# Optimization experiments

Measured on AMD Instinct MI355X. Metric: run time of the kernel, lower is better.

The kernel has to match this reference:

```python
import jax, jax.numpy as jnp
import numpy as np

B, S, H, E = 4, 2048, 2048, 8

def _gelu(x):
    return jax.nn.gelu(x, approximate=False)  # torch nn.GELU default (erf)

def setup_inputs() -> dict:
    key = jax.random.key(0)
    ks = jax.random.split(key, 12)
    sc = 1.0 / np.sqrt(H)
    inp = {
        'hidden_states': jax.random.normal(ks[0], (B, S, H), jnp.float32),
        'attention_mask': jnp.ones((B, S), jnp.float32),
        # operation detector: Linear(H,H) -> GELU -> Linear(H,8)
        'Wd1': jax.random.normal(ks[1], (H, H), jnp.float32) * sc,
        'bd1': jnp.zeros((H,), jnp.float32),
        'Wd2': jax.random.normal(ks[2], (H, E), jnp.float32) * sc,
        'bd2': jnp.zeros((E,), jnp.float32),
        # 8 expert handlers, each PrecisionAdaptiveLinear(H,H) -> stacked [E,H,H]
        'We': jax.random.normal(ks[3], (E, H, H), jnp.float32) * sc,
        'be': jnp.zeros((E, H), jnp.float32),
        # precision_integration: Linear(H,H) -> GELU -> Linear(H,H)
        'Wi1': jax.random.normal(ks[4], (H, H), jnp.float32) * sc,
        'bi1': jnp.zeros((H,), jnp.float32),
        'Wi2': jax.random.normal(ks[5], (H, H), jnp.float32) * sc,
        'bi2': jnp.zeros((H,), jnp.float32),
    }
    return inp

def _kahan_sum_last(x):
    # Numerically-stable Kahan summation over the last axis (E elements).
    s = jnp.zeros_like(x[..., 0])
    c = jnp.zeros_like(s)
    for i in range(x.shape[-1]):
        y = x[..., i] - c
        t = s + y
        c = (t - s) - y
        s = t
    return s

def reference(hidden_states, attention_mask, Wd1, bd1, Wd2, bd2, We, be, Wi1, bi1, Wi2, bi2):
    h = hidden_states
    # router: softmax over 8 operation logits (safe_softmax == stable softmax)
    logits = _gelu(h @ Wd1 + bd1) @ Wd2 + bd2            # [B,S,E]
    op_w = jax.nn.softmax(logits, axis=-1)               # [B,S,E]
    # all 8 expert linears as one batched GEMM: [B,S,E,H]
    expert_out = jnp.einsum('bsh,ehk->bsek', h, We) + be
    weighted = expert_out * op_w[:, :, :, None]          # [B,S,E,H]
    # Kahan-combine over experts (move E to last axis)
    combined = _kahan_sum_last(jnp.moveaxis(weighted, 2, -1))  # [B,S,H]
    enhanced = _gelu(combined @ Wi1 + bi1) @ Wi2 + bi2   # [B,S,H]
    enhanced = enhanced * attention_mask[:, :, None]
    return enhanced
```

## Files before the change

kernel.cpp:

```cpp
#include <hip/hip_runtime.h>
#include <hip/hip_bf16.h>


#define MTOT 8192
#define HDIM 2048

typedef short bf16x8 __attribute__((ext_vector_type(8)));
typedef float f32x4  __attribute__((ext_vector_type(4)));

__device__ __forceinline__ unsigned short f2bf(float x) {
    unsigned int u = __float_as_uint(x);
    unsigned int r = (u + 0x7FFFu + ((u >> 16) & 1u)) >> 16;
    return (unsigned short)r;
}
__device__ __forceinline__ float bf2f(unsigned short u) {
    return __uint_as_float(((unsigned int)u) << 16);
}
__device__ __forceinline__ float gelu_f(float x) {
    return 0.5f * x * (1.0f + erff(x * 0.70710678118654752f));
}

__global__ void k_split_x(const float* __restrict__ x,
                          unsigned short* __restrict__ hi,
                          unsigned short* __restrict__ lo, long n) {
    long i = ((long)blockIdx.x * blockDim.x + threadIdx.x) * 4;
    long stride = (long)gridDim.x * blockDim.x * 4;
    for (; i < n; i += stride) {
        float4 v = *reinterpret_cast<const float4*>(x + i);
        ushort4 h, l;
        h.x = f2bf(v.x); l.x = f2bf(v.x - bf2f(h.x));
        h.y = f2bf(v.y); l.y = f2bf(v.y - bf2f(h.y));
        h.z = f2bf(v.z); l.z = f2bf(v.z - bf2f(h.z));
        h.w = f2bf(v.w); l.w = f2bf(v.w - bf2f(h.w));
        *reinterpret_cast<ushort4*>(hi + i) = h;
        *reinterpret_cast<ushort4*>(lo + i) = l;
    }
}

__global__ void k_split_tr(const float* __restrict__ Wd1, const float* __restrict__ We,
                           const float* __restrict__ Wi1, const float* __restrict__ Wi2,
                           unsigned short* __restrict__ th, unsigned short* __restrict__ tl) {
    int z = blockIdx.z;
    const float* src = (z == 0) ? Wd1
                     : (z <= 8) ? (We + (size_t)(z - 1) * HDIM * HDIM)
                     : (z == 9) ? Wi1 : Wi2;
    size_t dof = (size_t)z * HDIM * HDIM;
    __shared__ float t[32][33];
    int n0 = blockIdx.x * 32, k0 = blockIdx.y * 32;
    int tx = threadIdx.x & 31, ty = threadIdx.x >> 5;
#pragma unroll
    for (int i = 0; i < 4; ++i) {
        int k = ty + i * 8;
        t[k][tx] = src[(size_t)(k0 + k) * HDIM + n0 + tx];
    }
    __syncthreads();
#pragma unroll
    for (int i = 0; i < 4; ++i) {
        int n = ty + i * 8;
        float v = t[tx][n];
        unsigned short hv = f2bf(v);
        unsigned short lv = f2bf(v - bf2f(hv));
        th[dof + (size_t)(n0 + n) * HDIM + k0 + tx] = hv;
        tl[dof + (size_t)(n0 + n) * HDIM + k0 + tx] = lv;
    }
}

__global__ void k_logits(const float* __restrict__ G1, const float* __restrict__ Wd2,
                         const float* __restrict__ bd2, float* __restrict__ opw) {
    int row = blockIdx.x * (blockDim.x >> 6) + (threadIdx.x >> 6);
    int lane = threadIdx.x & 63;
    if (row >= MTOT) return;
    const float* g = G1 + (size_t)row * HDIM;
    float a[8] = {0, 0, 0, 0, 0, 0, 0, 0};
    for (int k = lane; k < HDIM; k += 64) {
        float x = g[k];
        const float* w = Wd2 + (size_t)k * 8;
        float4 w0 = *reinterpret_cast<const float4*>(w);
        float4 w1 = *reinterpret_cast<const float4*>(w + 4);
        a[0] += x * w0.x; a[1] += x * w0.y; a[2] += x * w0.z; a[3] += x * w0.w;
        a[4] += x * w1.x; a[5] += x * w1.y; a[6] += x * w1.z; a[7] += x * w1.w;
    }
#pragma unroll
    for (int off = 32; off > 0; off >>= 1)
#pragma unroll
        for (int e = 0; e < 8; ++e) a[e] += __shfl_xor(a[e], off);
#pragma unroll
    for (int e = 0; e < 8; ++e) a[e] += bd2[e];
    float mx = a[0];
#pragma unroll
    for (int e = 1; e < 8; ++e) mx = fmaxf(mx, a[e]);
    float p[8], s = 0.f;
#pragma unroll
    for (int e = 0; e < 8; ++e) { p[e] = expf(a[e] - mx); s += p[e]; }
    float inv = 1.f / s;
    if (lane < 8) opw[(size_t)row * 8 + lane] = p[lane] * inv;
}

__device__ __forceinline__ void stage_tile(const unsigned short* __restrict__ g,
                                           unsigned short* l, int row0, int kt, int tid) {
    int wv = tid >> 6;
#pragma unroll
    for (int i = 0; i < 4; ++i) {
        int idx = i * 256 + tid;
        int row = idx >> 3;
        int chunk = (idx & 7) ^ (row & 7);
        const unsigned short* src = g + ((size_t)(row0 + row) << 11) + kt + (chunk << 3);
        unsigned short* dst = l + (size_t)((i * 256 + wv * 64) << 3);
        __builtin_amdgcn_global_load_lds((const __attribute__((address_space(1))) void*)src,
                                         (__attribute__((address_space(3))) void*)dst,
                                         16, 0, 0);
    }
}

__device__ __forceinline__ bf16x8 rd_frag(const unsigned short* l, int r, int kslot) {
    int slot = kslot ^ (r & 7);
    return *reinterpret_cast<const bf16x8*>(l + r * 64 + slot * 8);
}

#define MFMA3(ACC, AH, AL, BH, BL)                                              \
    ACC = __builtin_amdgcn_mfma_f32_16x16x32_bf16(AH, BH, ACC, 0, 0, 0);        \
    ACC = __builtin_amdgcn_mfma_f32_16x16x32_bf16(AH, BL, ACC, 0, 0, 0);        \
    ACC = __builtin_amdgcn_mfma_f32_16x16x32_bf16(AL, BH, ACC, 0, 0, 0);

template <int EPI>
__global__ __launch_bounds__(256, 2)
void k_gemm(const unsigned short* __restrict__ Ah, const unsigned short* __restrict__ Al,
            const unsigned short* __restrict__ Bh, const unsigned short* __restrict__ Bl,
            const float* __restrict__ bias, const float* __restrict__ mask,
            float* __restrict__ outF,
            unsigned short* __restrict__ oHi, unsigned short* __restrict__ oLo) {
    __shared__ unsigned short lds[4 * 8192];
    const int tid = threadIdx.x, lane = tid & 63, wv = tid >> 6;
    const int row0 = blockIdx.y * 128, col0 = blockIdx.x * 128;
    const int wm = wv >> 1, wn = wv & 1;
    f32x4 acc[4][4] = {};

    for (int kt = 0; kt < HDIM; kt += 64) {
        stage_tile(Ah, lds,          row0, kt, tid);
        stage_tile(Al, lds + 8192,   row0, kt, tid);
        stage_tile(Bh, lds + 16384,  col0, kt, tid);
        stage_tile(Bl, lds + 24576,  col0, kt, tid);
        __syncthreads();
#pragma unroll
        for (int kk = 0; kk < 2; ++kk) {
            const int ks = (kk << 2) + (lane >> 4);
            bf16x8 fah[4], fal[4], fbh[4], fbl[4];
#pragma unroll
            for (int m = 0; m < 4; ++m) {
                int r = wm * 64 + m * 16 + (lane & 15);
                fah[m] = rd_frag(lds, r, ks);
                fal[m] = rd_frag(lds + 8192, r, ks);
            }
#pragma unroll
            for (int n = 0; n < 4; ++n) {
                int c = wn * 64 + n * 16 + (lane & 15);
                fbh[n] = rd_frag(lds + 16384, c, ks);
                fbl[n] = rd_frag(lds + 24576, c, ks);
            }
#pragma unroll
            for (int m = 0; m < 4; ++m)
#pragma unroll
                for (int n = 0; n < 4; ++n) {
                    MFMA3(acc[m][n], fah[m], fal[m], fbh[n], fbl[n]);
                }
        }
        __syncthreads();
    }

#pragma unroll
    for (int m = 0; m < 4; ++m)
#pragma unroll
        for (int n = 0; n < 4; ++n) {
            int gc = col0 + wn * 64 + n * 16 + (lane & 15);
            float bv = bias[gc];
#pragma unroll
            for (int r = 0; r < 4; ++r) {
                int gr = row0 + wm * 64 + m * 16 + ((lane >> 4) << 2) + r;
                float v = acc[m][n][r] + bv;
                if constexpr (EPI == 0) {
                    outF[(size_t)gr * HDIM + gc] = gelu_f(v);
                } else if constexpr (EPI == 2) {
                    v = gelu_f(v);
                    unsigned short hv = f2bf(v), lv = f2bf(v - bf2f(hv));
                    oHi[(size_t)gr * HDIM + gc] = hv;
                    oLo[(size_t)gr * HDIM + gc] = lv;
                } else {
                    outF[(size_t)gr * HDIM + gc] = v * mask[gr];
                }
            }
        }
}

__global__ __launch_bounds__(256, 2)
void k_experts(const unsigned short* __restrict__ Xh, const unsigned short* __restrict__ Xl,
               const unsigned short* __restrict__ Wh, const unsigned short* __restrict__ Wl,
               const float* __restrict__ be, const float* __restrict__ opw,
               unsigned short* __restrict__ oHi, unsigned short* __restrict__ oLo) {
    __shared__ unsigned short lds[4 * 8192];
    const int tid = threadIdx.x, lane = tid & 63, wv = tid >> 6;
    const int row0 = blockIdx.y * 128, col0 = blockIdx.x * 128;
    const int wm = wv >> 1, wn = wv & 1;
    f32x4 accc[4][4] = {};

    for (int e = 0; e < 8; ++e) {
        const unsigned short* Bh = Wh + (size_t)e * HDIM * HDIM;
        const unsigned short* Bl = Wl + (size_t)e * HDIM * HDIM;
        f32x4 acc[4][4] = {};
        for (int kt = 0; kt < HDIM; kt += 64) {
            stage_tile(Xh, lds,          row0, kt, tid);
            stage_tile(Xl, lds + 8192,   row0, kt, tid);
            stage_tile(Bh, lds + 16384,  col0, kt, tid);
            stage_tile(Bl, lds + 24576,  col0, kt, tid);
            __syncthreads();
#pragma unroll
            for (int kk = 0; kk < 2; ++kk) {
                const int ks = (kk << 2) + (lane >> 4);
                bf16x8 fah[4], fal[4], fbh[4], fbl[4];
#pragma unroll
                for (int m = 0; m < 4; ++m) {
                    int r = wm * 64 + m * 16 + (lane & 15);
                    fah[m] = rd_frag(lds, r, ks);
                    fal[m] = rd_frag(lds + 8192, r, ks);
                }
#pragma unroll
                for (int n = 0; n < 4; ++n) {
                    int c = wn * 64 + n * 16 + (lane & 15);
                    fbh[n] = rd_frag(lds + 16384, c, ks);
                    fbl[n] = rd_frag(lds + 24576, c, ks);
                }
#pragma unroll
                for (int m = 0; m < 4; ++m)
#pragma unroll
                    for (int n = 0; n < 4; ++n) {
                        MFMA3(acc[m][n], fah[m], fal[m], fbh[n], fbl[n]);
                    }
            }
            __syncthreads();
        }
#pragma unroll
        for (int m = 0; m < 4; ++m)
#pragma unroll
            for (int r = 0; r < 4; ++r) {
                int gr = row0 + wm * 64 + m * 16 + ((lane >> 4) << 2) + r;
                float w = opw[(size_t)gr * 8 + e];
#pragma unroll
                for (int n = 0; n < 4; ++n) {
                    int gc = col0 + wn * 64 + n * 16 + (lane & 15);
                    accc[m][n][r] += w * (acc[m][n][r] + be[e * HDIM + gc]);
                }
            }
    }

#pragma unroll
    for (int m = 0; m < 4; ++m)
#pragma unroll
        for (int n = 0; n < 4; ++n) {
            int gc = col0 + wn * 64 + n * 16 + (lane & 15);
#pragma unroll
            for (int r = 0; r < 4; ++r) {
                int gr = row0 + wm * 64 + m * 16 + ((lane >> 4) << 2) + r;
                float v = accc[m][n][r];
                unsigned short hv = f2bf(v), lv = f2bf(v - bf2f(hv));
                oHi[(size_t)gr * HDIM + gc] = hv;
                oLo[(size_t)gr * HDIM + gc] = lv;
            }
        }
}

extern "C" void kernel_launch(void* const* d_in, const int* in_sizes, int n_in,
                              void* d_out, int out_size, void* d_ws, size_t ws_size,
                              hipStream_t stream) {
    const float* h    = (const float*)d_in[0];
    const float* amsk = (const float*)d_in[1];
    const float* Wd1  = (const float*)d_in[2];
    const float* bd1  = (const float*)d_in[3];
    const float* Wd2  = (const float*)d_in[4];
    const float* bd2  = (const float*)d_in[5];
    const float* We   = (const float*)d_in[6];
    const float* be   = (const float*)d_in[7];
    const float* Wi1  = (const float*)d_in[8];
    const float* bi1  = (const float*)d_in[9];
    const float* Wi2  = (const float*)d_in[10];
    const float* bi2  = (const float*)d_in[11];
    float* out = (float*)d_out;

    const size_t MB = 1ull << 20;
    char* ws = (char*)d_ws;
    unsigned short* Xh = (unsigned short*)(ws);
    unsigned short* Xl = (unsigned short*)(ws + 32 * MB);
    unsigned short* Wth = (unsigned short*)(ws + 64 * MB);
    unsigned short* Wtl = (unsigned short*)(ws + 152 * MB);
    char* rc = ws + 240 * MB;
    float*          G1  = (float*)rc;
    unsigned short* Chi = (unsigned short*)rc;
    unsigned short* Clo = (unsigned short*)(rc + 32 * MB);
    float* opw = (float*)(ws + 304 * MB);
    unsigned short* Thi = Xh;
    unsigned short* Tlo = Xl;

    const size_t WMAT = (size_t)HDIM * HDIM;
    dim3 gemm_grid(HDIM / 128, MTOT / 128);

    k_split_x<<<4096, 256, 0, stream>>>(h, Xh, Xl, (long)MTOT * HDIM);
    k_split_tr<<<dim3(64, 64, 11), 256, 0, stream>>>(Wd1, We, Wi1, Wi2, Wth, Wtl);
    k_gemm<0><<<gemm_grid, 256, 0, stream>>>(Xh, Xl, Wth, Wtl, bd1, nullptr,
                                             G1, nullptr, nullptr);
    k_logits<<<MTOT / 4, 256, 0, stream>>>(G1, Wd2, bd2, opw);
    k_experts<<<gemm_grid, 256, 0, stream>>>(Xh, Xl, Wth + WMAT, Wtl + WMAT,
                                             be, opw, Chi, Clo);
    k_gemm<2><<<gemm_grid, 256, 0, stream>>>(Chi, Clo, Wth + 9 * WMAT, Wtl + 9 * WMAT,
                                             bi1, nullptr, nullptr, Thi, Tlo);
    k_gemm<3><<<gemm_grid, 256, 0, stream>>>(Thi, Tlo, Wth + 10 * WMAT, Wtl + 10 * WMAT,
                                             bi2, amsk, out, nullptr, nullptr);
}
```

Baseline: 2.119 ms.

## Unify GEMMs into 256x256 double-buffered kernel with interleaved expert accumulation

Replaces the 128x128 GEMM and the separate expert kernel with one templated 512-thread kernel using 256x256 tiles, K-step 32, and double-buffered LDS staging that overlaps global loads with MFMA. For the expert stage, the K loop is interleaved across the 8 experts so each A tile is loaded once and reused by all experts. A single accumulator is rescaled by ratios of router weights (w[e-1]/w[e]), so the weighted expert sum needs no per-expert accumulators. This raises register and LDS pressure, drops the XOR swizzle (risking bank conflicts), and the weight-ratio trick can become inaccurate or divide by zero for tiny softmax weights.

```diff
diff --git a/kernel.cpp b/kernel.cpp
--- a/kernel.cpp
+++ b/kernel.cpp
@@ -4,16 +4,17 @@
 
 #define MTOT 8192
 #define HDIM 2048
+#define WMAT ((size_t)HDIM * HDIM)
 
 typedef short bf16x8 __attribute__((ext_vector_type(8)));
 typedef float f32x4  __attribute__((ext_vector_type(4)));
-
-__device__ __forceinline__ unsigned short f2bf(float x) {
+typedef unsigned short u16;
+
+__device__ __forceinline__ u16 f2bf(float x) {
     unsigned int u = __float_as_uint(x);
-    unsigned int r = (u + 0x7FFFu + ((u >> 16) & 1u)) >> 16;
-    return (unsigned short)r;
-}
-__device__ __forceinline__ float bf2f(unsigned short u) {
+    return (u16)((u + 0x7FFFu + ((u >> 16) & 1u)) >> 16);
+}
+__device__ __forceinline__ float bf2f(u16 u) {
     return __uint_as_float(((unsigned int)u) << 16);
 }
 __device__ __forceinline__ float gelu_f(float x) {
@@ -21,8 +22,7 @@
 }
 
 __global__ void k_split_x(const float* __restrict__ x,
-                          unsigned short* __restrict__ hi,
-                          unsigned short* __restrict__ lo, long n) {
+                          u16* __restrict__ hi, u16* __restrict__ lo, long n) {
     long i = ((long)blockIdx.x * blockDim.x + threadIdx.x) * 4;
     long stride = (long)gridDim.x * blockDim.x * 4;
     for (; i < n; i += stride) {
@@ -39,12 +39,12 @@
 
 __global__ void k_split_tr(const float* __restrict__ Wd1, const float* __restrict__ We,
                            const float* __restrict__ Wi1, const float* __restrict__ Wi2,
-                           unsigned short* __restrict__ th, unsigned short* __restrict__ tl) {
+                           u16* __restrict__ th, u16* __restrict__ tl) {
     int z = blockIdx.z;
     const float* src = (z == 0) ? Wd1
-                     : (z <= 8) ? (We + (size_t)(z - 1) * HDIM * HDIM)
+                     : (z <= 8) ? (We + (size_t)(z - 1) * WMAT)
                      : (z == 9) ? Wi1 : Wi2;
-    size_t dof = (size_t)z * HDIM * HDIM;
+    size_t dof = (size_t)z * WMAT;
     __shared__ float t[32][33];
     int n0 = blockIdx.x * 32, k0 = blockIdx.y * 32;
     int tx = threadIdx.x & 31, ty = threadIdx.x >> 5;
@@ -58,8 +58,7 @@
     for (int i = 0; i < 4; ++i) {
         int n = ty + i * 8;
         float v = t[tx][n];
-        unsigned short hv = f2bf(v);
-        unsigned short lv = f2bf(v - bf2f(hv));
+        u16 hv = f2bf(v), lv = f2bf(v - bf2f(hv));
         th[dof + (size_t)(n0 + n) * HDIM + k0 + tx] = hv;
         tl[dof + (size_t)(n0 + n) * HDIM + k0 + tx] = lv;
     }
@@ -96,175 +95,159 @@
     if (lane < 8) opw[(size_t)row * 8 + lane] = p[lane] * inv;
 }
 
-__device__ __forceinline__ void stage_tile(const unsigned short* __restrict__ g,
-                                           unsigned short* l, int row0, int kt, int tid) {
+__device__ __forceinline__ void stage_tile32(const u16* __restrict__ g, size_t row0,
+                                             int k0, u16* dst, int tid) {
     int wv = tid >> 6;
 #pragma unroll
-    for (int i = 0; i < 4; ++i) {
-        int idx = i * 256 + tid;
-        int row = idx >> 3;
-        int chunk = (idx & 7) ^ (row & 7);
-        const unsigned short* src = g + ((size_t)(row0 + row) << 11) + kt + (chunk << 3);
-        unsigned short* dst = l + (size_t)((i * 256 + wv * 64) << 3);
+    for (int i = 0; i < 2; ++i) {
+        int slot = i * 512 + tid;
+        int row = slot >> 2, chunk = slot & 3;
+        const u16* src = g + (row0 + (size_t)row) * HDIM + k0 + chunk * 8;
+        u16* d = dst + (size_t)((i * 512 + wv * 64) << 3);
         __builtin_amdgcn_global_load_lds((const __attribute__((address_space(1))) void*)src,
-                                         (__attribute__((address_space(3))) void*)dst,
+                                         (__attribute__((address_space(3))) void*)d,
                                          16, 0, 0);
     }
 }
 
-__device__ __forceinline__ bf16x8 rd_frag(const unsigned short* l, int r, int kslot) {
-    int slot = kslot ^ (r & 7);
-    return *reinterpret_cast<const bf16x8*>(l + r * 64 + slot * 8);
-}
-
-#define MFMA3(ACC, AH, AL, BH, BL)                                              \
-    ACC = __builtin_amdgcn_mfma_f32_16x16x32_bf16(AH, BH, ACC, 0, 0, 0);        \
-    ACC = __builtin_amdgcn_mfma_f32_16x16x32_bf16(AH, BL, ACC, 0, 0, 0);        \
-    ACC = __builtin_amdgcn_mfma_f32_16x16x32_bf16(AL, BH, ACC, 0, 0, 0);
-
-template <int EPI>
-__global__ __launch_bounds__(256, 2)
-void k_gemm(const unsigned short* __restrict__ Ah, const unsigned short* __restrict__ Al,
-            const unsigned short* __restrict__ Bh, const unsigned short* __restrict__ Bl,
-            const float* __restrict__ bias, const float* __restrict__ mask,
-            float* __restrict__ outF,
-            unsigned short* __restrict__ oHi, unsigned short* __restrict__ oLo) {
-    __shared__ unsigned short lds[4 * 8192];
+template <int NE, int EPI>
+__global__ __launch_bounds__(512, 2)
+void k_mm(const u16* __restrict__ Ah, const u16* __restrict__ Al,
+          const u16* __restrict__ Bh, const u16* __restrict__ Bl,
+          const float* __restrict__ opw, const float* __restrict__ bias,
+          const float* __restrict__ mask, float* __restrict__ outF,
+          u16* __restrict__ oHi, u16* __restrict__ oLo) {
+    __shared__ u16 lsA[2][2][256 * 32];
+    __shared__ u16 lsB[2][2][256 * 32];
+    __shared__ float rat[NE == 8 ? 256 * 8 : 8];
+
     const int tid = threadIdx.x, lane = tid & 63, wv = tid >> 6;
-    const int row0 = blockIdx.y * 128, col0 = blockIdx.x * 128;
+    const int bx = blockIdx.x & 7, by = blockIdx.x >> 3;
+    const size_t row0 = (size_t)by * 256, col0 = (size_t)bx * 256;
     const int wm = wv >> 1, wn = wv & 1;
-    f32x4 acc[4][4] = {};
-
-    for (int kt = 0; kt < HDIM; kt += 64) {
-        stage_tile(Ah, lds,          row0, kt, tid);
-        stage_tile(Al, lds + 8192,   row0, kt, tid);
-        stage_tile(Bh, lds + 16384,  col0, kt, tid);
-        stage_tile(Bl, lds + 24576,  col0, kt, tid);
+    const int lp = lane & 15, lq = lane >> 4;
+
+    if (NE == 8 && tid < 256) {
+        const float* w = opw + (row0 + tid) * 8;
+        float w8[8];
+#pragma unroll
+        for (int e = 0; e < 8; ++e) w8[e] = w[e];
+#pragma unroll
+        for (int e = 0; e < 8; ++e) rat[tid * 8 + e] = w8[(e + 7) & 7] / w8[e];
+    }
+
+    stage_tile32(Ah, row0, 0, lsA[0][0], tid);
+    stage_tile32(Al, row0, 0, lsA[0][1], tid);
+    stage_tile32(Bh, col0, 0, lsB[0][0], tid);
+    stage_tile32(Bl, col0, 0, lsB[0][1], tid);
+    __syncthreads();
+
+    f32x4 acc[4][8] = {};
+    const int NS = NE * (HDIM / 32);
+    int ab = 0, bb = 0;
+
+    for (int s = 0; s < NS; ++s) {
+        const int e = s & (NE - 1);
+        const int s1 = s + 1;
+        if (s1 < NS) {
+            const int e1 = s1 & (NE - 1);
+            const int k1 = (s1 / NE) * 32;
+            if (e1 == 0) {
+                stage_tile32(Ah, row0, k1, lsA[ab ^ 1][0], tid);
+                stage_tile32(Al, row0, k1, lsA[ab ^ 1][1], tid);
+            }
+            stage_tile32(Bh + (size_t)e1 * WMAT, col0, k1, lsB[bb ^ 1][0], tid);
+            stage_tile32(Bl + (size_t)e1 * WMAT, col0, k1, lsB[bb ^ 1][1], tid);
+        }
+        if (NE == 8 && s > 0) {
+#pragma unroll
+            for (int m = 0; m < 4; ++m)
+#pragma unroll
+                for (int r = 0; r < 4; ++r) {
+                    float rv = rat[(wm * 64 + m * 16 + lq * 4 + r) * 8 + e];
+#pragma unroll
+                    for (int n = 0; n < 8; ++n) acc[m][n][r] *= rv;
+                }
+        }
+        bf16x8 fah[4], fal[4];
+#pragma unroll
+        for (int m = 0; m < 4; ++m) {
+            int rr = wm * 64 + m * 16 + lp;
+            fah[m] = *(const bf16x8*)(lsA[ab][0] + rr * 32 + lq * 8);
+            fal[m] = *(const bf16x8*)(lsA[ab][1] + rr * 32 + lq * 8);
+        }
+#pragma unroll
+        for (int n = 0; n < 8; ++n) {
+            int cr = wn * 128 + n * 16 + lp;
+            bf16x8 fbh = *(const bf16x8*)(lsB[bb][0] + cr * 32 + lq * 8);
+            bf16x8 fbl = *(const bf16x8*)(lsB[bb][1] + cr * 32 + lq * 8);
+#pragma unroll
+            for (int m = 0; m < 4; ++m) {
+                acc[m][n] = __builtin_amdgcn_mfma_f32_16x16x32_bf16(fah[m], fbh, acc[m][n], 0, 0, 0);
+                acc[m][n] = __builtin_amdgcn_mfma_f32_16x16x32_bf16(fah[m], fbl, acc[m][n], 0, 0, 0);
+                acc[m][n] = __builtin_amdgcn_mfma_f32_16x16x32_bf16(fal[m], fbh, acc[m][n], 0, 0, 0);
+            }
+        }
         __syncthreads();
-#pragma unroll
-        for (int kk = 0; kk < 2; ++kk) {
-            const int ks = (kk << 2) + (lane >> 4);
-            bf16x8 fah[4], fal[4], fbh[4], fbl[4];
-#pragma unroll
-            for (int m = 0; m < 4; ++m) {
-                int r = wm * 64 + m * 16 + (lane & 15);
-                fah[m] = rd_frag(lds, r, ks);
-                fal[m] = rd_frag(lds + 8192, r, ks);
-            }
-#pragma unroll
-            for (int n = 0; n < 4; ++n) {
-                int c = wn * 64 + n * 16 + (lane & 15);
-                fbh[n] = rd_frag(lds + 16384, c, ks);
-                fbl[n] = rd_frag(lds + 24576, c, ks);
-            }
-#pragma unroll
-            for (int m = 0; m < 4; ++m)
-#pragma unroll
-                for (int n = 0; n < 4; ++n) {
-                    MFMA3(acc[m][n], fah[m], fal[m], fbh[n], fbl[n]);
-                }
-        }
-        __syncthreads();
-    }
-
-#pragma unroll
-    for (int m = 0; m < 4; ++m)
-#pragma unroll
-        for (int n = 0; n < 4; ++n) {
-            int gc = col0 + wn * 64 + n * 16 + (lane & 15);
-            float bv = bias[gc];
+        if (s1 < NS) {
+            if ((s1 & (NE - 1)) == 0) ab ^= 1;
+            bb ^= 1;
+        }
+    }
+
+    if constexpr (EPI == 1) {
+        float bev[8][8];
+#pragma unroll
+        for (int n = 0; n < 8; ++n) {
+            size_t gc = col0 + wn * 128 + n * 16 + lp;
+#pragma unroll
+            for (int e = 0; e < 8; ++e) bev[n][e] = bias[(size_t)e * HDIM + gc];
+        }
+#pragma unroll
+        for (int m = 0; m < 4; ++m)
 #pragma unroll
             for (int r = 0; r < 4; ++r) {
-                int gr = row0 + wm * 64 + m * 16 + ((lane >> 4) << 2) + r;
-                float v = acc[m][n][r] + bv;
-                if constexpr (EPI == 0) {
-                    outF[(size_t)gr * HDIM + gc] = gelu_f(v);
-                } else if constexpr (EPI == 2) {
-                    v = gelu_f(v);
-                    unsigned short hv = f2bf(v), lv = f2bf(v - bf2f(hv));
-                    oHi[(size_t)gr * HDIM + gc] = hv;
-                    oLo[(size_t)gr * HDIM + gc] = lv;
-                } else {
-                    outF[(size_t)gr * HDIM + gc] = v * mask[gr];
+                size_t gr = row0 + wm * 64 + m * 16 + lq * 4 + r;
+                const float* w = opw + gr * 8;
+                float w8[8];
+#pragma unroll
+                for (int e = 0; e < 8; ++e) w8[e] = w[e];
+#pragma unroll
+                for (int n = 0; n < 8; ++n) {
+                    float bsum = 0.f;
+#pragma unroll
+                    for (int e = 0; e < 8; ++e) bsum += w8[e] * bev[n][e];
+                    float v = acc[m][n][r] * w8[7] + bsum;
+                    size_t gc = col0 + wn * 128 + n * 16 + lp;
+                    u16 hv = f2bf(v), lv = f2bf(v - bf2f(hv));
+                    oHi[gr * HDIM + gc] = hv;
+                    oLo[gr * HDIM + gc] = lv;
                 }
             }
-        }
-}
-
-__global__ __launch_bounds__(256, 2)
-void k_experts(const unsigned short* __restrict__ Xh, const unsigned short* __restrict__ Xl,
-               const unsigned short* __restrict__ Wh, const unsigned short* __restrict__ Wl,
-               const float* __restrict__ be, const float* __restrict__ opw,
-               unsigned short* __restrict__ oHi, unsigned short* __restrict__ oLo) {
-    __shared__ unsigned short lds[4 * 8192];
-    const int tid = threadIdx.x, lane = tid & 63, wv = tid >> 6;
-    const int row0 = blockIdx.y * 128, col0 = blockIdx.x * 128;
-    const int wm = wv >> 1, wn = wv & 1;
-    f32x4 accc[4][4] = {};
-
-    for (int e = 0; e < 8; ++e) {
-        const unsigned short* Bh = Wh + (size_t)e * HDIM * HDIM;
-        const unsigned short* Bl = Wl + (size_t)e * HDIM * HDIM;
-        f32x4 acc[4][4] = {};
-        for (int kt = 0; kt < HDIM; kt += 64) {
-            stage_tile(Xh, lds,          row0, kt, tid);
-            stage_tile(Xl, lds + 8192,   row0, kt, tid);
-            stage_tile(Bh, lds + 16384,  col0, kt, tid);
-            stage_tile(Bl, lds + 24576,  col0, kt, tid);
-            __syncthreads();
-#pragma unroll
-            for (int kk = 0; kk < 2; ++kk) {
-                const int ks = (kk << 2) + (lane >> 4);
-                bf16x8 fah[4], fal[4], fbh[4], fbl[4];
-#pragma unroll
-                for (int m = 0; m < 4; ++m) {
-                    int r = wm * 64 + m * 16 + (lane & 15);
-                    fah[m] = rd_frag(lds, r, ks);
-                    fal[m] = rd_frag(lds + 8192, r, ks);
+    } else {
+#pragma unroll
+        for (int n = 0; n < 8; ++n) {
+            size_t gc = col0 + wn * 128 + n * 16 + lp;
+            float bv = bias[gc];
+#pragma unroll
+            for (int m = 0; m < 4; ++m)
+#pragma unroll
+                for (int r = 0; r < 4; ++r) {
+                    size_t gr = row0 + wm * 64 + m * 16 + lq * 4 + r;
+                    float v = acc[m][n][r] + bv;
+                    if constexpr (EPI == 0) {
+                        outF[gr * HDIM + gc] = gelu_f(v);
+                    } else if constexpr (EPI == 2) {
+                        v = gelu_f(v);
+                        u16 hv = f2bf(v), lv = f2bf(v - bf2f(hv));
+                        oHi[gr * HDIM + gc] = hv;
+                        oLo[gr * HDIM + gc] = lv;
+                    } else {
+                        outF[gr * HDIM + gc] = v * mask[gr];
+                    }
                 }
-#pragma unroll
-                for (int n = 0; n < 4; ++n) {
-                    int c = wn * 64 + n * 16 + (lane & 15);
-                    fbh[n] = rd_frag(lds + 16384, c, ks);
-                    fbl[n] = rd_frag(lds + 24576, c, ks);
-                }
-#pragma unroll
-                for (int m = 0; m < 4; ++m)
-#pragma unroll
-                    for (int n = 0; n < 4; ++n) {
-                        MFMA3(acc[m][n], fah[m], fal[m], fbh[n], fbl[n]);
-                    }
-            }
-            __syncthreads();
-        }
-#pragma unroll
-        for (int m = 0; m < 4; ++m)
-#pragma unroll
-            for (int r = 0; r < 4; ++r) {
-                int gr = row0 + wm * 64 + m * 16 + ((lane >> 4) << 2) + r;
-                float w = opw[(size_t)gr * 8 + e];
-#pragma unroll
-                for (int n = 0; n < 4; ++n) {
-                    int gc = col0 + wn * 64 + n * 16 + (lane & 15);
-                    accc[m][n][r] += w * (acc[m][n][r] + be[e * HDIM + gc]);
-                }
-            }
-    }
-
-#pragma unroll
-    for (int m = 0; m < 4; ++m)
-#pragma unroll
-        for (int n = 0; n < 4; ++n) {
-            int gc = col0 + wn * 64 + n * 16 + (lane & 15);
-#pragma unroll
-            for (int r = 0; r < 4; ++r) {
-                int gr = row0 + wm * 64 + m * 16 + ((lane >> 4) << 2) + r;
-                float v = accc[m][n][r];
-                unsigned short hv = f2bf(v), lv = f2bf(v - bf2f(hv));
-                oHi[(size_t)gr * HDIM + gc] = hv;
-                oLo[(size_t)gr * HDIM + gc] = lv;
-            }
-        }
+        }
+    }
 }
 
 extern "C" void kernel_launch(void* const* d_in, const int* in_sizes, int n_in,
@@ -286,30 +269,28 @@
 
     const size_t MB = 1ull << 20;
     char* ws = (char*)d_ws;
-    unsigned short* Xh = (unsigned short*)(ws);
-    unsigned short* Xl = (unsigned short*)(ws + 32 * MB);
-    unsigned short* Wth = (unsigned short*)(ws + 64 * MB);
-    unsigned short* Wtl = (unsigned short*)(ws + 152 * MB);
+    u16* Xh = (u16*)(ws);
+    u16* Xl = (u16*)(ws + 32 * MB);
+    u16* Wth = (u16*)(ws + 64 * MB);
+    u16* Wtl = (u16*)(ws + 152 * MB);
     char* rc = ws + 240 * MB;
-    float*          G1  = (float*)rc;
-    unsigned short* Chi = (unsigned short*)rc;
-    unsigned short* Clo = (unsigned short*)(rc + 32 * MB);
+    float* G1  = (float*)rc;
+    u16*   Chi = (u16*)rc;
+    u16*   Clo = (u16*)(rc + 32 * MB);
     float* opw = (float*)(ws + 304 * MB);
-    unsigned short* Thi = Xh;
-    unsigned short* Tlo = Xl;
-
-    const size_t WMAT = (size_t)HDIM * HDIM;
-    dim3 gemm_grid(HDIM / 128, MTOT / 128);
+    u16* Thi = Xh;
+    u16* Tlo = Xl;
 
     k_split_x<<<4096, 256, 0, stream>>>(h, Xh, Xl, (long)MTOT * HDIM);
     k_split_tr<<<dim3(64, 64, 11), 256, 0, stream>>>(Wd1, We, Wi1, Wi2, Wth, Wtl);
-    k_gemm<0><<<gemm_grid, 256, 0, stream>>>(Xh, Xl, Wth, Wtl, bd1, nullptr,
-                                             G1, nullptr, nullptr);
+
+    k_mm<1, 0><<<256, 512, 0, stream>>>(Xh, Xl, Wth, Wtl, nullptr, bd1, nullptr,
+                                        G1, nullptr, nullptr);
     k_logits<<<MTOT / 4, 256, 0, stream>>>(G1, Wd2, bd2, opw);
-    k_experts<<<gemm_grid, 256, 0, stream>>>(Xh, Xl, Wth + WMAT, Wtl + WMAT,
-                                             be, opw, Chi, Clo);
-    k_gemm<2><<<gemm_grid, 256, 0, stream>>>(Chi, Clo, Wth + 9 * WMAT, Wtl + 9 * WMAT,
-                                             bi1, nullptr, nullptr, Thi, Tlo);
-    k_gemm<3><<<gemm_grid, 256, 0, stream>>>(Thi, Tlo, Wth + 10 * WMAT, Wtl + 10 * WMAT,
-                                             bi2, amsk, out, nullptr, nullptr);
-}
+    k_mm<8, 1><<<256, 512, 0, stream>>>(Xh, Xl, Wth + WMAT, Wtl + WMAT, opw, be,
+                                        nullptr, nullptr, Chi, Clo);
+    k_mm<1, 2><<<256, 512, 0, stream>>>(Chi, Clo, Wth + 9 * WMAT, Wtl + 9 * WMAT,
+                                        nullptr, bi1, nullptr, nullptr, Thi, Tlo);
+    k_mm<1, 3><<<256, 512, 0, stream>>>(Thi, Tlo, Wth + 10 * WMAT, Wtl + 10 * WMAT,
+                                        nullptr, bi2, amsk, out, nullptr, nullptr);
+}
```

Result: slower. 2.441 ms (+15.2%).
